# Kernel tuning notes

Measured on AMD Instinct MI355X. Metric: run time of the kernel, lower is better.

## Reference

```python
import jax, jax.numpy as jnp
import numpy as np

NEG = -10000.0
START, STOP = 4, 5
NT = 6  # 4 emotions + START + STOP
B, T, V = 512, 2048, 100000


def setup_inputs():
    key = jax.random.key(0)
    ks = jax.random.split(key, 7)
    transitions = jax.random.normal(ks[0], (NT, NT), jnp.float32)
    transitions = transitions.at[START, :].set(NEG).at[:, STOP].set(NEG)
    weight_for_emo_shift = jax.random.normal(ks[1], (4,), jnp.float32)
    multiplier = jax.random.normal(ks[2], (4, 4), jnp.float32)
    multiplier = multiplier.at[jnp.arange(4), jnp.arange(4)].set(NEG)
    out_table = jax.random.normal(ks[3], (V, 4), jnp.float32)
    bias = jax.random.uniform(ks[4], (B, T), jnp.float32)
    sentence = jax.random.randint(ks[5], (B, T), 0, V)
    tags = jax.random.randint(ks[6], (B, T), 0, 4)
    return {"transitions": transitions, "weight_for_emo_shift": weight_for_emo_shift,
            "multiplier": multiplier, "out_table": out_table, "bias": bias,
            "sentence": sentence, "tags": tags}


def _feats(out_table, sentence):
    # sentence: [T] int -> feats [T, 6]; cols 0..3 from out_table lookup,
    # col 4 = +3 at first turn else -3, col 5 = +3 at last turn else -3.
    t = sentence.shape[0]
    emo = out_table[sentence]                                      # [T,4]
    col4 = jnp.full((t,), -3.0, out_table.dtype).at[0].set(3.0)
    col5 = jnp.full((t,), -3.0, out_table.dtype).at[t - 1].set(3.0)
    return jnp.concatenate([emo, col4[:, None], col5[:, None]], axis=1)


def _nll_one(transitions, w, M, feats, bias, tags):
    # CRF forward algorithm (log-partition) minus gold path score for one dialog.
    t = feats.shape[0]

    def step(alpha, inp):
        feat, b = inp                                              # feat [6], b scalar
        shift = b * jnp.tanh((b - 0.5) * w)                        # [4]
        te = transitions.at[:4, :4].add(M * shift[None, :])        # [next, prev]
        alpha = jax.nn.logsumexp(alpha[None, :] + te, axis=1) + feat
        return alpha, None

    alpha0 = jnp.full((NT,), NEG, feats.dtype).at[START].set(0.0)
    alphaT, _ = jax.lax.scan(step, alpha0, (feats, bias))
    fwd = jax.nn.logsumexp(alphaT + transitions[STOP])

    # gold score
    prev = jnp.concatenate([jnp.array([START], tags.dtype), tags[:-1]])
    pc = jnp.clip(prev, 0, 3)
    ar = jnp.arange(t)
    shift = bias[:, None] * jnp.tanh((bias[:, None] - 0.5) * w[None, :])  # [T,4]
    biased = shift[ar, pc] * M[tags, pc]
    use_bias = (tags < 4) & (prev < 4)
    trans_s = transitions[tags, prev] + jnp.where(use_bias, biased, 0.0)
    gold = jnp.sum(trans_s + feats[ar, tags]) + transitions[STOP, tags[-1]]
    return fwd - gold


def reference(transitions, weight_for_emo_shift, multiplier, out_table, bias, sentence, tags):
    # multiplier: softmax over dim 0, then diagonal forced to -1 (as in the
    # in-place .data mutations in the original loop).
    M = jax.nn.softmax(multiplier, axis=0)
    M = M.at[jnp.arange(4), jnp.arange(4)].set(-1.0)
    feats = jax.vmap(lambda s: _feats(out_table, s))(sentence)     # [B,T,6]
    nll = jax.vmap(lambda f, b, tg: _nll_one(transitions, weight_for_emo_shift, M, f, b, tg))(feats, bias, tags)
    return nll                                                     # [B]
```

## Files before the change

### kernel.cpp

```cpp
#include <hip/hip_runtime.h>
#include <hip/hip_fp16.h>

#define TT 2048
#define BB 512

typedef __fp16 h2 __attribute__((ext_vector_type(2)));

#if __has_builtin(__builtin_amdgcn_exp2f)
__device__ __forceinline__ float fexp2(float x){ return __builtin_amdgcn_exp2f(x); }
#else
__device__ __forceinline__ float fexp2(float x){ return exp2f(x); }
#endif
#if __has_builtin(__builtin_amdgcn_logf)
__device__ __forceinline__ float flog2(float x){ return __builtin_amdgcn_logf(x); }
#else
__device__ __forceinline__ float flog2(float x){ return log2f(x); }
#endif
__device__ __forceinline__ float frcp(float x){ return __builtin_amdgcn_rcpf(x); }

__device__ __forceinline__ float lse2_4(float x0,float x1,float x2,float x3){
  float m = fmaxf(fmaxf(x0,x1),fmaxf(x2,x3));
  float e = fexp2(x0-m)+fexp2(x1-m)+fexp2(x2-m)+fexp2(x3-m);
  return m + flog2(e);
}

__global__ __launch_bounds__(512, 4) void crf_kernel(
    const float* __restrict__ trans,
    const float* __restrict__ w,
    const float* __restrict__ mult,
    const float* __restrict__ out_table,
    const float* __restrict__ bias,
    const int*   __restrict__ sentence,
    const int*   __restrict__ tags,
    float* __restrict__ out)
{
  constexpr float INVLN2 = 1.4426950408889634f;
  constexpr float LN2    = 0.6931471805599453f;
  const int b   = blockIdx.x;
  const int tid = threadIdx.x;

  __shared__ __align__(16) char s_te[65536];
  __shared__ float s_PAm[128*16];
  __shared__ float s_PAs[128*4];
  __shared__ float s_M[16];
  __shared__ float s_wgold[8];
  float* s_PBm = (float*)s_te;
  float* s_PBs = (float*)(s_te + 4096);

  float trans2[16];
  #pragma unroll
  for (int i=0;i<4;i++)
    #pragma unroll
    for (int k=0;k<4;k++)
      trans2[i*4+k] = trans[i*6+k]*INVLN2;

  float M[16];
  {
    float e[16]; float cs[4]={0.f,0.f,0.f,0.f};
    #pragma unroll
    for (int i=0;i<4;i++)
      #pragma unroll
      for (int j=0;j<4;j++){
        float v = fexp2(mult[i*4+j]*INVLN2);
        e[i*4+j] = v; cs[j] += v;
      }
    #pragma unroll
    for (int j=0;j<4;j++) cs[j] = frcp(cs[j]);
    #pragma unroll
    for (int i=0;i<4;i++)
      #pragma unroll
      for (int j=0;j<4;j++)
        M[i*4+j] = (i==j) ? -1.f : e[i*4+j]*cs[j];
  }
  const float w0=w[0], w1=w[1], w2=w[2], w3=w[3];
  if (tid==0){
    #pragma unroll
    for (int i=0;i<16;i++) s_M[i]=M[i];
  }
  __syncthreads();

  float gold = 0.f;
  #pragma unroll 2
  for (int r=0;r<4;r++){
    int t    = tid + (r<<9);
    int base = b*TT + t;
    float bb = bias[base];
    int sent = sentence[base];
    int tg   = tags[base];
    float4 f4 = *reinterpret_cast<const float4*>(out_table + (size_t)sent*4);

    const float c2 = 2.f*INVLN2;
    float y0 = fexp2((bb-0.5f)*w0*c2); float sa = bb*(y0-1.f)*frcp(y0+1.f);
    float y1 = fexp2((bb-0.5f)*w1*c2); float sb = bb*(y1-1.f)*frcp(y1+1.f);
    float y2 = fexp2((bb-0.5f)*w2*c2); float sc = bb*(y2-1.f)*frcp(y2+1.f);
    float y3 = fexp2((bb-0.5f)*w3*c2); float sd = bb*(y3-1.f)*frcp(y3+1.f);

    float sh2[4] = {sa*INVLN2, sb*INVLN2, sc*INVLN2, sd*INVLN2};
    float f2[4]  = {f4.x*INVLN2, f4.y*INVLN2, f4.z*INVLN2, f4.w*INVLN2};

    float e[16];
    #pragma unroll
    for (int i=0;i<4;i++)
      #pragma unroll
      for (int k=0;k<4;k++)
        e[i*4+k] = fexp2(fmaf(M[i*4+k], sh2[k], trans2[i*4+k] + f2[i]));
    if (t==0){
      #pragma unroll
      for (int i=0;i<16;i++) e[i] = 0.f;
      e[0]=e[5]=e[10]=e[15]=1.f;
    }
    h2 tp[8];
    #pragma unroll
    for (int q=0;q<8;q++) tp[q] = __builtin_amdgcn_cvt_pkrtz(e[2*q], e[2*q+1]);
    int K = (t>>5)&7;
    int g = (t ^ K) << 4;
    *(float4*)(s_te + g)         = *(float4*)&tp[0];
    *(float4*)(s_te + 32768 + g) = *(float4*)&tp[4];

    float term;
    if (t==0){
      term = trans[tg*6+4];
    } else {
      int pv = tags[base-1];
      float shp = (pv==0)?sa:(pv==1)?sb:(pv==2)?sc:sd;
      term = trans[tg*6+pv] + shp * s_M[tg*4+pv];
    }
    term += (tg==0)?f4.x:(tg==1)?f4.y:(tg==2)?f4.z:f4.w;
    if (t==TT-1) term += trans[30+tg];
    gold += term;
  }
  #pragma unroll
  for (int off=32; off>0; off>>=1) gold += __shfl_down(gold, off);
  if ((tid & 63)==0) s_wgold[tid>>6] = gold;
  __syncthreads();

  {
    int c = tid>>2, j = tid&3;
    int t0 = c<<4;
    int K  = (t0>>5)&7;
    float p0=(j==0)?1.f:0.f, p1=(j==1)?1.f:0.f, p2=(j==2)?1.f:0.f, p3=(j==3)?1.f:0.f;
    float L = 0.f;
    #pragma unroll 4
    for (int s=0;s<16;s++){
      int g = ((t0+s) ^ K) << 4;
      float4 q0 = *(const float4*)(s_te + g);
      float4 q1 = *(const float4*)(s_te + 32768 + g);
      const h2* ha = (const h2*)&q0;
      const h2* hb = (const h2*)&q1;
      float n0 = fmaf((float)ha[0][0], p0, (float)ha[0][1] * p1);
      n0 = fmaf((float)ha[1][0], p2, n0); n0 = fmaf((float)ha[1][1], p3, n0);
      float n1 = fmaf((float)ha[2][0], p0, (float)ha[2][1] * p1);
      n1 = fmaf((float)ha[3][0], p2, n1); n1 = fmaf((float)ha[3][1], p3, n1);
      float n2 = fmaf((float)hb[0][0], p0, (float)hb[0][1] * p1);
      n2 = fmaf((float)hb[1][0], p2, n2); n2 = fmaf((float)hb[1][1], p3, n2);
      float n3 = fmaf((float)hb[2][0], p0, (float)hb[2][1] * p1);
      n3 = fmaf((float)hb[3][0], p2, n3); n3 = fmaf((float)hb[3][1], p3, n3);
      p0=n0; p1=n1; p2=n2; p3=n3;
      if ((s&7)==7){
        float sum = (p0+p1)+(p2+p3);
        float inv = frcp(sum);
        L += flog2(sum);
        p0*=inv; p1*=inv; p2*=inv; p3*=inv;
      }
    }
    s_PAm[c*16 + 0*4 + j] = p0;
    s_PAm[c*16 + 1*4 + j] = p1;
    s_PAm[c*16 + 2*4 + j] = p2;
    s_PAm[c*16 + 3*4 + j] = p3;
    s_PAs[c*4 + j] = L;
  }
  __syncthreads();

  float *srcM = s_PAm, *srcS = s_PAs, *dstM = s_PBm, *dstS = s_PBs;
  #pragma unroll 1
  for (int n=64; n>=1; n>>=1){
    if (tid < n*4){
      int p = tid>>2, j = tid&3;
      const float* Am = srcM + (2*p)*16;
      const float* As = srcS + (2*p)*4;
      const float* Bm = Am + 16;
      const float* Bs = As + 4;
      float b0=Bs[0], b1=Bs[1], b2=Bs[2], b3=Bs[3];
      float m = fmaxf(fmaxf(b0,b1), fmaxf(b2,b3));
      float a0 = Am[0*4+j]*fexp2(b0-m);
      float a1 = Am[1*4+j]*fexp2(b1-m);
      float a2 = Am[2*4+j]*fexp2(b2-m);
      float a3 = Am[3*4+j]*fexp2(b3-m);
      float c0 = fmaf(Bm[ 0],a0, fmaf(Bm[ 1],a1, fmaf(Bm[ 2],a2, Bm[ 3]*a3)));
      float c1 = fmaf(Bm[ 4],a0, fmaf(Bm[ 5],a1, fmaf(Bm[ 6],a2, Bm[ 7]*a3)));
      float c2 = fmaf(Bm[ 8],a0, fmaf(Bm[ 9],a1, fmaf(Bm[10],a2, Bm[11]*a3)));
      float c3 = fmaf(Bm[12],a0, fmaf(Bm[13],a1, fmaf(Bm[14],a2, Bm[15]*a3)));
      float ssum = fmaxf((c0+c1)+(c2+c3), 1e-37f);
      float inv = frcp(ssum);
      dstM[p*16+0*4+j] = c0*inv;
      dstM[p*16+1*4+j] = c1*inv;
      dstM[p*16+2*4+j] = c2*inv;
      dstM[p*16+3*4+j] = c3*inv;
      dstS[p*4+j] = m + As[j] + flog2(ssum);
    }
    __syncthreads();
    float* tm;
    tm=srcM; srcM=dstM; dstM=tm;
    tm=srcS; srcS=dstS; dstS=tm;
  }

  if (tid==0){
    const float* Pf = srcM;
    const float* Ls = srcS;
    int s0 = sentence[b*TT];
    float4 f0 = *reinterpret_cast<const float4*>(out_table + (size_t)s0*4);
    float a0 = (trans[ 4] + f0.x)*INVLN2;
    float a1 = (trans[10] + f0.y)*INVLN2;
    float a2 = (trans[16] + f0.z)*INVLN2;
    float a3 = (trans[22] + f0.w)*INVLN2;
    float u0 = Ls[0]+a0, u1 = Ls[1]+a1, u2 = Ls[2]+a2, u3 = Ls[3]+a3;
    float m2 = fmaxf(fmaxf(u0,u1), fmaxf(u2,u3));
    float e0 = fexp2(u0-m2), e1 = fexp2(u1-m2), e2 = fexp2(u2-m2), e3 = fexp2(u3-m2);
    float v0 = fmaf(Pf[ 0],e0, fmaf(Pf[ 1],e1, fmaf(Pf[ 2],e2, Pf[ 3]*e3)));
    float v1 = fmaf(Pf[ 4],e0, fmaf(Pf[ 5],e1, fmaf(Pf[ 6],e2, Pf[ 7]*e3)));
    float v2 = fmaf(Pf[ 8],e0, fmaf(Pf[ 9],e1, fmaf(Pf[10],e2, Pf[11]*e3)));
    float v3 = fmaf(Pf[12],e0, fmaf(Pf[13],e1, fmaf(Pf[14],e2, Pf[15]*e3)));
    float n0 = flog2(v0)+m2, n1 = flog2(v1)+m2, n2 = flog2(v2)+m2, n3 = flog2(v3)+m2;
    float fwd2 = lse2_4(n0+trans[30]*INVLN2, n1+trans[31]*INVLN2,
                        n2+trans[32]*INVLN2, n3+trans[33]*INVLN2);
    float g = ((s_wgold[0]+s_wgold[1])+(s_wgold[2]+s_wgold[3]))
            + ((s_wgold[4]+s_wgold[5])+(s_wgold[6]+s_wgold[7]));
    out[b] = fwd2*LN2 - g;
  }
}

extern "C" void kernel_launch(void* const* d_in, const int* in_sizes, int n_in,
                              void* d_out, int out_size, void* d_ws, size_t ws_size,
                              hipStream_t stream) {
  const float* trans     = (const float*)d_in[0];
  const float* w         = (const float*)d_in[1];
  const float* mult      = (const float*)d_in[2];
  const float* out_table = (const float*)d_in[3];
  const float* bias      = (const float*)d_in[4];
  const int*   sentence  = (const int*)d_in[5];
  const int*   tags      = (const int*)d_in[6];
  crf_kernel<<<BB, 512, 0, stream>>>(trans, w, mult, out_table, bias, sentence, tags,
                                     (float*)d_out);
}
```

Measured before the change: 20.00 us.

## Store per-step transition matrices as FP8 with per-step scaling offsets

Per-step exponentiated transition matrices now go to LDS as 8-bit floats instead of fp16. Each step is shifted by a scaling offset so its values fit FP8 range, and the offsets are stored separately and added back into the log-scale during the chunk scan. This halves LDS footprint and traffic. Loads are also vectorized: each thread handles 4 consecutive timesteps with float4/int4 loads, and the previous tag comes from a shuffle. FP8 (3 mantissa bits) adds significant rounding error to the log-partition, which risks failing the accuracy tolerance.

```diff
diff --git a/kernel.cpp b/kernel.cpp
--- a/kernel.cpp
+++ b/kernel.cpp
@@ -1,10 +1,7 @@
 #include <hip/hip_runtime.h>
-#include <hip/hip_fp16.h>
 
 #define TT 2048
 #define BB 512
-
-typedef __fp16 h2 __attribute__((ext_vector_type(2)));
 
 #if __has_builtin(__builtin_amdgcn_exp2f)
 __device__ __forceinline__ float fexp2(float x){ return __builtin_amdgcn_exp2f(x); }
@@ -17,6 +14,43 @@
 __device__ __forceinline__ float flog2(float x){ return log2f(x); }
 #endif
 __device__ __forceinline__ float frcp(float x){ return __builtin_amdgcn_rcpf(x); }
+
+#if __has_builtin(__builtin_amdgcn_cvt_pk_fp8_f32) && __has_builtin(__builtin_amdgcn_cvt_pk_f32_fp8)
+__device__ __forceinline__ unsigned enc_lo(float a,float b,unsigned old){
+  return (unsigned)__builtin_amdgcn_cvt_pk_fp8_f32(a,b,(int)old,false);
+}
+__device__ __forceinline__ unsigned enc_hi(float a,float b,unsigned old){
+  return (unsigned)__builtin_amdgcn_cvt_pk_fp8_f32(a,b,(int)old,true);
+}
+__device__ __forceinline__ void dec_lo(unsigned w,float&x,float&y){
+  auto r=__builtin_amdgcn_cvt_pk_f32_fp8((int)w,false); x=r[0]; y=r[1];
+}
+__device__ __forceinline__ void dec_hi(unsigned w,float&x,float&y){
+  auto r=__builtin_amdgcn_cvt_pk_f32_fp8((int)w,true); x=r[0]; y=r[1];
+}
+#else
+__device__ __forceinline__ unsigned enc1(float x){
+  if (!(x > 0x1p-10f)) return 0u;
+  unsigned b = __float_as_uint(x) + 0x80000u;
+  int e = (int)((b>>23)&0xFF) - 127;
+  if (e < -6){ int m = (int)(x*512.0f + 0.5f); return (unsigned)m; }
+  if (e > 8) return 0x7Eu;
+  return (unsigned)(((e+7)<<3) | ((b>>20)&7));
+}
+__device__ __forceinline__ float dec1(unsigned byte){
+  unsigned e=(byte>>3)&0xF, m=byte&7;
+  if (e==0) return (float)m * 0x1p-9f;
+  return __uint_as_float(((e+120u)<<23)|(m<<20));
+}
+__device__ __forceinline__ unsigned enc_lo(float a,float b,unsigned old){
+  return (old & 0xFFFF0000u) | enc1(a) | (enc1(b)<<8);
+}
+__device__ __forceinline__ unsigned enc_hi(float a,float b,unsigned old){
+  return (old & 0x0000FFFFu) | (enc1(a)<<16) | (enc1(b)<<24);
+}
+__device__ __forceinline__ void dec_lo(unsigned w,float&x,float&y){ x=dec1(w&0xFF); y=dec1((w>>8)&0xFF); }
+__device__ __forceinline__ void dec_hi(unsigned w,float&x,float&y){ x=dec1((w>>16)&0xFF); y=dec1(w>>24); }
+#endif
 
 __device__ __forceinline__ float lse2_4(float x0,float x1,float x2,float x3){
   float m = fmaxf(fmaxf(x0,x1),fmaxf(x2,x3));
@@ -39,20 +73,25 @@
   const int b   = blockIdx.x;
   const int tid = threadIdx.x;
 
-  __shared__ __align__(16) char s_te[65536];
+  __shared__ __align__(16) char  s_te[32768];
+  __shared__ __align__(16) float s_c[2048];
   __shared__ float s_PAm[128*16];
   __shared__ float s_PAs[128*4];
   __shared__ float s_M[16];
+  __shared__ float s_tr[36];
   __shared__ float s_wgold[8];
   float* s_PBm = (float*)s_te;
-  float* s_PBs = (float*)(s_te + 4096);
-
-  float trans2[16];
+  float* s_PBs = (float*)(s_te + 16384);
+
+  float trans2[16]; float t2max = -1e30f;
   #pragma unroll
   for (int i=0;i<4;i++)
     #pragma unroll
-    for (int k=0;k<4;k++)
-      trans2[i*4+k] = trans[i*6+k]*INVLN2;
+    for (int k=0;k<4;k++){
+      float v = trans[i*6+k]*INVLN2;
+      trans2[i*4+k] = v; t2max = fmaxf(t2max, v);
+    }
+  const float T144 = t2max + 1.4427f;
 
   float M[16];
   {
@@ -62,17 +101,19 @@
       #pragma unroll
       for (int j=0;j<4;j++){
         float v = fexp2(mult[i*4+j]*INVLN2);
-        e[i*4+j] = v; cs[j] += v;
+        e[i*4+j]=v; cs[j]+=v;
       }
     #pragma unroll
-    for (int j=0;j<4;j++) cs[j] = frcp(cs[j]);
+    for (int j=0;j<4;j++) cs[j]=frcp(cs[j]);
     #pragma unroll
     for (int i=0;i<4;i++)
       #pragma unroll
       for (int j=0;j<4;j++)
         M[i*4+j] = (i==j) ? -1.f : e[i*4+j]*cs[j];
   }
-  const float w0=w[0], w1=w[1], w2=w[2], w3=w[3];
+  const float wc0=w[0]*2.f*INVLN2, wc1=w[1]*2.f*INVLN2,
+              wc2=w[2]*2.f*INVLN2, wc3=w[3]*2.f*INVLN2;
+  if (tid<36) s_tr[tid]=trans[tid];
   if (tid==0){
     #pragma unroll
     for (int i=0;i<16;i++) s_M[i]=M[i];
@@ -80,54 +121,82 @@
   __syncthreads();
 
   float gold = 0.f;
-  #pragma unroll 2
-  for (int r=0;r<4;r++){
-    int t    = tid + (r<<9);
-    int base = b*TT + t;
-    float bb = bias[base];
-    int sent = sentence[base];
-    int tg   = tags[base];
-    float4 f4 = *reinterpret_cast<const float4*>(out_table + (size_t)sent*4);
-
-    const float c2 = 2.f*INVLN2;
-    float y0 = fexp2((bb-0.5f)*w0*c2); float sa = bb*(y0-1.f)*frcp(y0+1.f);
-    float y1 = fexp2((bb-0.5f)*w1*c2); float sb = bb*(y1-1.f)*frcp(y1+1.f);
-    float y2 = fexp2((bb-0.5f)*w2*c2); float sc = bb*(y2-1.f)*frcp(y2+1.f);
-    float y3 = fexp2((bb-0.5f)*w3*c2); float sd = bb*(y3-1.f)*frcp(y3+1.f);
-
-    float sh2[4] = {sa*INVLN2, sb*INVLN2, sc*INVLN2, sd*INVLN2};
-    float f2[4]  = {f4.x*INVLN2, f4.y*INVLN2, f4.z*INVLN2, f4.w*INVLN2};
-
-    float e[16];
-    #pragma unroll
-    for (int i=0;i<4;i++)
-      #pragma unroll
-      for (int k=0;k<4;k++)
-        e[i*4+k] = fexp2(fmaf(M[i*4+k], sh2[k], trans2[i*4+k] + f2[i]));
-    if (t==0){
-      #pragma unroll
-      for (int i=0;i<16;i++) e[i] = 0.f;
-      e[0]=e[5]=e[10]=e[15]=1.f;
-    }
-    h2 tp[8];
-    #pragma unroll
-    for (int q=0;q<8;q++) tp[q] = __builtin_amdgcn_cvt_pkrtz(e[2*q], e[2*q+1]);
-    int K = (t>>5)&7;
-    int g = (t ^ K) << 4;
-    *(float4*)(s_te + g)         = *(float4*)&tp[0];
-    *(float4*)(s_te + 32768 + g) = *(float4*)&tp[4];
-
-    float term;
-    if (t==0){
-      term = trans[tg*6+4];
-    } else {
-      int pv = tags[base-1];
-      float shp = (pv==0)?sa:(pv==1)?sb:(pv==2)?sc:sd;
-      term = trans[tg*6+pv] + shp * s_M[tg*4+pv];
-    }
-    term += (tg==0)?f4.x:(tg==1)?f4.y:(tg==2)?f4.z:f4.w;
-    if (t==TT-1) term += trans[30+tg];
-    gold += term;
+  {
+    const int t0   = tid<<2;
+    const int base = b*TT + t0;
+    float4 bb4 = *reinterpret_cast<const float4*>(bias + base);
+    int4  sen4 = *reinterpret_cast<const int4*>(sentence + base);
+    int4  tg4  = *reinterpret_cast<const int4*>(tags + base);
+    float4 ft0 = *reinterpret_cast<const float4*>(out_table + (size_t)sen4.x*4);
+    float4 ft1 = *reinterpret_cast<const float4*>(out_table + (size_t)sen4.y*4);
+    float4 ft2 = *reinterpret_cast<const float4*>(out_table + (size_t)sen4.z*4);
+    float4 ft3 = *reinterpret_cast<const float4*>(out_table + (size_t)sen4.w*4);
+
+    int pv0 = __shfl_up(tg4.w, 1);
+    if ((tid & 63)==0 && t0>0) pv0 = tags[base-1];
+
+    float cv[4];
+    #pragma unroll
+    for (int e=0;e<4;e++){
+      const int t = t0 + e;
+      float bb   = (e==0)?bb4.x:(e==1)?bb4.y:(e==2)?bb4.z:bb4.w;
+      float4 f4e = (e==0)?ft0:(e==1)?ft1:(e==2)?ft2:ft3;
+      int tg     = (e==0)?tg4.x:(e==1)?tg4.y:(e==2)?tg4.z:tg4.w;
+
+      float bh = bb-0.5f;
+      float y0=fexp2(bh*wc0); float sh0=bb*(y0-1.f)*frcp(y0+1.f);
+      float y1=fexp2(bh*wc1); float sh1=bb*(y1-1.f)*frcp(y1+1.f);
+      float y2=fexp2(bh*wc2); float sh2v=bb*(y2-1.f)*frcp(y2+1.f);
+      float y3=fexp2(bh*wc3); float sh3=bb*(y3-1.f)*frcp(y3+1.f);
+      float s20=sh0*INVLN2, s21=sh1*INVLN2, s22=sh2v*INVLN2, s23=sh3*INVLN2;
+      float f20=f4e.x*INVLN2, f21=f4e.y*INVLN2, f22=f4e.z*INVLN2, f23=f4e.w*INVLN2;
+
+      float ct  = fmaxf(fmaxf(f20,f21),fmaxf(f22,f23)) + T144;
+      float off = 8.0f - ct;
+      float o0=f20+off, o1=f21+off, o2=f22+off, o3=f23+off;
+      float a00=fexp2(fmaf(M[ 0],s20,trans2[ 0]+o0));
+      float a01=fexp2(fmaf(M[ 1],s21,trans2[ 1]+o0));
+      float a02=fexp2(fmaf(M[ 2],s22,trans2[ 2]+o0));
+      float a03=fexp2(fmaf(M[ 3],s23,trans2[ 3]+o0));
+      float a10=fexp2(fmaf(M[ 4],s20,trans2[ 4]+o1));
+      float a11=fexp2(fmaf(M[ 5],s21,trans2[ 5]+o1));
+      float a12=fexp2(fmaf(M[ 6],s22,trans2[ 6]+o1));
+      float a13=fexp2(fmaf(M[ 7],s23,trans2[ 7]+o1));
+      float a20=fexp2(fmaf(M[ 8],s20,trans2[ 8]+o2));
+      float a21=fexp2(fmaf(M[ 9],s21,trans2[ 9]+o2));
+      float a22=fexp2(fmaf(M[10],s22,trans2[10]+o2));
+      float a23=fexp2(fmaf(M[11],s23,trans2[11]+o2));
+      float a30=fexp2(fmaf(M[12],s20,trans2[12]+o3));
+      float a31=fexp2(fmaf(M[13],s21,trans2[13]+o3));
+      float a32=fexp2(fmaf(M[14],s22,trans2[14]+o3));
+      float a33=fexp2(fmaf(M[15],s23,trans2[15]+o3));
+
+      unsigned d0=enc_lo(a00,a01,0u); d0=enc_hi(a02,a03,d0);
+      unsigned d1=enc_lo(a10,a11,0u); d1=enc_hi(a12,a13,d1);
+      unsigned d2=enc_lo(a20,a21,0u); d2=enc_hi(a22,a23,d2);
+      unsigned d3=enc_lo(a30,a31,0u); d3=enc_hi(a32,a33,d3);
+      int K=(t>>5)&7; int g=(t^K)<<4;
+      *reinterpret_cast<uint4*>(s_te+g) = make_uint4(d0,d1,d2,d3);
+      cv[e]=ct;
+
+      int pv = (e==0)?pv0:((e==1)?tg4.x:(e==2)?tg4.y:tg4.z);
+      float term;
+      if (t==0){
+        term = s_tr[tg*6+4];
+      } else {
+        float shp=(pv==0)?sh0:(pv==1)?sh1:(pv==2)?sh2v:sh3;
+        term = s_tr[tg*6+pv] + shp*s_M[tg*4+pv];
+      }
+      term += (tg==0)?f4e.x:(tg==1)?f4e.y:(tg==2)?f4e.z:f4e.w;
+      if (t==TT-1) term += s_tr[30+tg];
+      gold += term;
+    }
+    *reinterpret_cast<float4*>(reinterpret_cast<char*>(s_c)+(t0<<2)) =
+        make_float4(cv[0],cv[1],cv[2],cv[3]);
+    if (tid==0){
+      *reinterpret_cast<uint4*>(s_te) = make_uint4(0x38u,0x3800u,0x380000u,0x38000000u);
+      s_c[0] = 8.0f;
+    }
   }
   #pragma unroll
   for (int off=32; off>0; off>>=1) gold += __shfl_down(gold, off);
@@ -136,33 +205,37 @@
 
   {
     int c = tid>>2, j = tid&3;
-    int t0 = c<<4;
-    int K  = (t0>>5)&7;
+    int t0c = c<<4;
+    int K  = (t0c>>5)&7;
     float p0=(j==0)?1.f:0.f, p1=(j==1)?1.f:0.f, p2=(j==2)?1.f:0.f, p3=(j==3)?1.f:0.f;
     float L = 0.f;
-    #pragma unroll 4
+    #pragma unroll
     for (int s=0;s<16;s++){
-      int g = ((t0+s) ^ K) << 4;
-      float4 q0 = *(const float4*)(s_te + g);
-      float4 q1 = *(const float4*)(s_te + 32768 + g);
-      const h2* ha = (const h2*)&q0;
-      const h2* hb = (const h2*)&q1;
-      float n0 = fmaf((float)ha[0][0], p0, (float)ha[0][1] * p1);
-      n0 = fmaf((float)ha[1][0], p2, n0); n0 = fmaf((float)ha[1][1], p3, n0);
-      float n1 = fmaf((float)ha[2][0], p0, (float)ha[2][1] * p1);
-      n1 = fmaf((float)ha[3][0], p2, n1); n1 = fmaf((float)ha[3][1], p3, n1);
-      float n2 = fmaf((float)hb[0][0], p0, (float)hb[0][1] * p1);
-      n2 = fmaf((float)hb[1][0], p2, n2); n2 = fmaf((float)hb[1][1], p3, n2);
-      float n3 = fmaf((float)hb[2][0], p0, (float)hb[2][1] * p1);
-      n3 = fmaf((float)hb[3][0], p2, n3); n3 = fmaf((float)hb[3][1], p3, n3);
+      int g = ((t0c+s) ^ K) << 4;
+      uint4 q = *reinterpret_cast<const uint4*>(s_te + g);
+      float e0,e1,e2,e3;
+      dec_lo(q.x,e0,e1); dec_hi(q.x,e2,e3);
+      float n0 = fmaf(e0,p0, e1*p1); n0 = fmaf(e2,p2,n0); n0 = fmaf(e3,p3,n0);
+      dec_lo(q.y,e0,e1); dec_hi(q.y,e2,e3);
+      float n1 = fmaf(e0,p0, e1*p1); n1 = fmaf(e2,p2,n1); n1 = fmaf(e3,p3,n1);
+      dec_lo(q.z,e0,e1); dec_hi(q.z,e2,e3);
+      float n2 = fmaf(e0,p0, e1*p1); n2 = fmaf(e2,p2,n2); n2 = fmaf(e3,p3,n2);
+      dec_lo(q.w,e0,e1); dec_hi(q.w,e2,e3);
+      float n3 = fmaf(e0,p0, e1*p1); n3 = fmaf(e2,p2,n3); n3 = fmaf(e3,p3,n3);
       p0=n0; p1=n1; p2=n2; p3=n3;
       if ((s&7)==7){
-        float sum = (p0+p1)+(p2+p3);
+        float sum = fmaxf((p0+p1)+(p2+p3), 1e-30f);
         float inv = frcp(sum);
         L += flog2(sum);
         p0*=inv; p1*=inv; p2*=inv; p3*=inv;
       }
     }
+    const float4* cp = reinterpret_cast<const float4*>(
+        reinterpret_cast<const char*>(s_c)+(t0c<<2));
+    float4 ca=cp[0], cb=cp[1], cc=cp[2], cd=cp[3];
+    L += ((ca.x+ca.y+ca.z+ca.w)+(cb.x+cb.y+cb.z+cb.w))
+       + ((cc.x+cc.y+cc.z+cc.w)+(cd.x+cd.y+cd.z+cd.w)) - 128.0f;
+
     s_PAm[c*16 + 0*4 + j] = p0;
     s_PAm[c*16 + 1*4 + j] = p1;
     s_PAm[c*16 + 2*4 + j] = p2;
```

Result: no change. 20.13 us (+0.6%).
